# Kernel optimization log

Measured on AMD Instinct MI355X. Metric: run time of the kernel, lower is better.

The kernel has to match this reference:

```python
import jax, jax.numpy as jnp
import numpy as np

M = 2048      # tokens (batch*seq)
K = 4096      # infeatures
N = 4096      # outfeatures
G = 128       # quantization groupsize


def setup_inputs() -> dict:
    key = jax.random.key(0)
    k1, k2, k3 = jax.random.split(key, 3)
    x = jax.random.normal(k1, (M, K), dtype=jnp.float32)
    # Packed int4 weights: 8 nibbles per int32. Row block i holds output
    # features 8*i..8*i+7 for every input feature (tile=1 layout).
    B = jax.random.randint(k2, (N // 8, K), 0, 2**31 - 1, dtype=jnp.int32)
    # Per-group symmetric scales, shape (K//G, N); small positive values.
    s = jax.random.uniform(k3, (K // G, N), dtype=jnp.float32, minval=0.005, maxval=0.02)
    return {"x": x, "B": B, "s": s}


def reference(x, B, s):
    # Unpack 8 4-bit values per int32: nibble r of B[i, j] is weight
    # for output feature 8*i + r, input feature j.
    shifts = (jnp.arange(8, dtype=jnp.int32) * 4)
    nib = (B[:, None, :] >> shifts[None, :, None]) & 0xF        # (N//8, 8, K)
    w = nib.reshape(N, K).astype(jnp.float32) - 8.0              # symmetric: q - (maxq+1)/2
    # Scale for weight (n_idx, k_idx) is s[k_idx // G, n_idx].
    scale = jnp.repeat(s, G, axis=0).T                           # (N, K)
    w_dq = w * scale                                             # dequantized weight
    return x @ w_dq.T                                            # (M, N)
```

## Files before the change

kernel.cpp:

```cpp
#include <hip/hip_runtime.h>
#include <stdint.h>
#include <stddef.h>

#define MDIM 2048
#define KDIM 4096
#define NDIM 4096
#define NTILE 32

using i32x4  = __attribute__((ext_vector_type(4))) int;
using i32x16 = __attribute__((ext_vector_type(16))) int;
using c16    = __attribute__((ext_vector_type(16))) char;

#define QA 31.75f
#define QW 793.75f
#define OUT_SCALE 3.9680203e-5f

__device__ __forceinline__ int q8(float v) {
    float r = rintf(v);
    r = fmaxf(-127.f, fminf(127.f, r));
    return (int)r;
}

__global__ __launch_bounds__(256) void prep(const float* __restrict__ x,
                                            const int* __restrict__ Bq,
                                            const float* __restrict__ s,
                                            char* __restrict__ a8,
                                            char* __restrict__ w8) {
    const int b = blockIdx.x, tid = threadIdx.x;
    if (b < 2048) {
        size_t t = (size_t)b * 256 + tid;
        const float* p = x + t * 16;
        float4 v0 = *(const float4*)(p);
        float4 v1 = *(const float4*)(p + 4);
        float4 v2 = *(const float4*)(p + 8);
        float4 v3 = *(const float4*)(p + 12);
        c16 o;
        o[0]  = (char)q8(v0.x * QA); o[1]  = (char)q8(v0.y * QA);
        o[2]  = (char)q8(v0.z * QA); o[3]  = (char)q8(v0.w * QA);
        o[4]  = (char)q8(v1.x * QA); o[5]  = (char)q8(v1.y * QA);
        o[6]  = (char)q8(v1.z * QA); o[7]  = (char)q8(v1.w * QA);
        o[8]  = (char)q8(v2.x * QA); o[9]  = (char)q8(v2.y * QA);
        o[10] = (char)q8(v2.z * QA); o[11] = (char)q8(v2.w * QA);
        o[12] = (char)q8(v3.x * QA); o[13] = (char)q8(v3.y * QA);
        o[14] = (char)q8(v3.z * QA); o[15] = (char)q8(v3.w * QA);
        *(c16*)(a8 + t * 16) = o;
    } else {
        const int n8 = b - 2048;
        const int kc = tid;
        const int* p = Bq + (size_t)n8 * KDIM + kc * 16;
        int v[16];
        {
            int4 b0 = *(const int4*)(p);
            int4 b1 = *(const int4*)(p + 4);
            int4 b2 = *(const int4*)(p + 8);
            int4 b3 = *(const int4*)(p + 12);
            v[0]=b0.x; v[1]=b0.y; v[2]=b0.z; v[3]=b0.w;
            v[4]=b1.x; v[5]=b1.y; v[6]=b1.z; v[7]=b1.w;
            v[8]=b2.x; v[9]=b2.y; v[10]=b2.z; v[11]=b2.w;
            v[12]=b3.x; v[13]=b3.y; v[14]=b3.z; v[15]=b3.w;
        }
        const float* sp = s + (size_t)(kc >> 3) * NDIM + n8 * 8;
        float4 s0 = *(const float4*)(sp);
        float4 s1 = *(const float4*)(sp + 4);
        float scv[8] = { s0.x * QW, s0.y * QW, s0.z * QW, s0.w * QW,
                         s1.x * QW, s1.y * QW, s1.z * QW, s1.w * QW };
#pragma unroll
        for (int r = 0; r < 8; ++r) {
            const int sh = r * 4;
            const float sc = scv[r];
            c16 o;
#pragma unroll
            for (int e = 0; e < 16; ++e)
                o[e] = (char)q8((float)(((v[e] >> sh) & 0xF) - 8) * sc);
            *(c16*)(w8 + (size_t)(n8 * 8 + r) * KDIM + kc * 16) = o;
        }
    }
}

__device__ __forceinline__ void gload16(const char* g, char* l) {
    __builtin_amdgcn_global_load_lds(
        (const __attribute__((address_space(1))) uint32_t*)g,
        (__attribute__((address_space(3))) uint32_t*)l, 16, 0, 0);
}

__global__ __launch_bounds__(256, 2) void gemm_i8(const char* __restrict__ A,
                                                  const char* __restrict__ W,
                                                  float* __restrict__ C) {
    __shared__ __align__(16) char L[2][2][2][8192];

    const int tid  = threadIdx.x;
    const int lane = tid & 63;
    const int wave = tid >> 6;

    const int wg    = blockIdx.y * gridDim.x + blockIdx.x;
    const int xcd   = wg & 7;
    const int local = wg >> 3;
    const int bx    = xcd * 4 + (local & 3);
    const int by    = local >> 2;
    const int bm = by * 128;
    const int bn = bx * 128;

    const int wm = (wave >> 1) * 64;
    const int wn = (wave & 1) * 64;
    const int r32 = lane & 31;
    const int hi  = lane >> 5;

    const int sr0 = tid & 127,  sq0 = tid >> 7;
    const int sr1 = sr0,        sq1 = sq0 + 2;
    const size_t a0 = (size_t)(bm + sr0) * KDIM + sq0 * 16;
    const size_t a1 = (size_t)(bm + sr1) * KDIM + sq1 * 16;
    const size_t w0 = (size_t)(bn + sr0) * KDIM + sq0 * 16;
    const size_t w1 = (size_t)(bn + sr1) * KDIM + sq1 * 16;
    const int d0 = tid * 16, d1 = d0 + 4096;

    int asl[2][2], bsl[2][2];
#pragma unroll
    for (int i = 0; i < 2; i++)
#pragma unroll
        for (int kk = 0; kk < 2; kk++) {
            asl[i][kk] = (kk * 2 + hi) * 2048 + (wm + i * 32 + r32) * 16;
            bsl[i][kk] = (kk * 2 + hi) * 2048 + (wn + i * 32 + r32) * 16;
        }

    i32x16 acc[2][2] = {};

#define STAGE(SB, SK, KT) do {                                               \
        const size_t kb_ = (size_t)(KT) * 128 + (SK) * 64;                   \
        gload16(A + a0 + kb_, &L[SB][SK][0][d0]);                            \
        gload16(A + a1 + kb_, &L[SB][SK][0][d1]);                            \
        gload16(W + w0 + kb_, &L[SB][SK][1][d0]);                            \
        gload16(W + w1 + kb_, &L[SB][SK][1][d1]);                            \
    } while (0)

    STAGE(0, 0, 0);
    STAGE(0, 1, 0);
    asm volatile("s_waitcnt vmcnt(0)" ::: "memory");
    __builtin_amdgcn_s_barrier();

    for (int t = 0; t < NTILE; ++t) {
        const int buf = t & 1;
        const int nt  = (t + 1 < NTILE) ? t + 1 : NTILE - 1;
        const int nb  = (t + 1) & 1;
        STAGE(nb, 0, nt);
        STAGE(nb, 1, nt);

        i32x4 af[2][2][2], bf[2][2][2];
#pragma unroll
        for (int s = 0; s < 2; ++s) {
#pragma unroll
            for (int i = 0; i < 2; i++)
#pragma unroll
                for (int kk = 0; kk < 2; kk++) {
                    af[s][i][kk] = *(const i32x4*)&L[buf][s][0][asl[i][kk]];
                    bf[s][i][kk] = *(const i32x4*)&L[buf][s][1][bsl[i][kk]];
                }
        }

        __builtin_amdgcn_s_setprio(1);
#pragma unroll
        for (int s = 0; s < 2; ++s)
#pragma unroll
            for (int kk = 0; kk < 2; kk++)
#pragma unroll
                for (int i = 0; i < 2; i++)
#pragma unroll
                    for (int j = 0; j < 2; j++)
                        acc[i][j] = __builtin_amdgcn_mfma_i32_32x32x32_i8(
                            af[s][i][kk], bf[s][j][kk], acc[i][j], 0, 0, 0);
        __builtin_amdgcn_s_setprio(0);

        asm volatile("s_waitcnt vmcnt(0)" ::: "memory");
        __builtin_amdgcn_s_barrier();
    }
#undef STAGE

    const int colb = bn + wn + r32;
#pragma unroll
    for (int i = 0; i < 2; i++)
#pragma unroll
        for (int j = 0; j < 2; j++)
#pragma unroll
            for (int g = 0; g < 16; ++g) {
                const int row = bm + wm + i * 32 + (g & 3) + 8 * (g >> 2) + 4 * hi;
                C[(size_t)row * NDIM + (colb + j * 32)]
                    = (float)acc[i][j][g] * OUT_SCALE;
            }
}

extern "C" void kernel_launch(void* const* d_in, const int* in_sizes, int n_in,
                              void* d_out, int out_size, void* d_ws, size_t ws_size,
                              hipStream_t stream) {
    const float* x  = (const float*)d_in[0];
    const int*   Bq = (const int*)d_in[1];
    const float* s  = (const float*)d_in[2];
    float* out = (float*)d_out;

    char* a8 = (char*)d_ws;
    char* w8 = a8 + (size_t)MDIM * KDIM;

    hipLaunchKernelGGL(prep, dim3(2560), dim3(256), 0, stream,
                       x, Bq, s, a8, w8);
    hipLaunchKernelGGL(gemm_i8, dim3(NDIM / 128, MDIM / 128), dim3(256),
                       0, stream, a8, w8, out);
}
```

Baseline: 167.6 us.

## Pre-tile int8 operands into LDS-ready panel layout for contiguous GEMM loads

The prep kernel now writes quantized activations and weights in a tiled panel layout: 128-row panels split into 64-wide K slices, each an 8 KB block already laid out exactly as the GEMM's LDS staging expects. The GEMM then loads each slice with fully contiguous 16-byte global_load_lds accesses instead of strided row reads across a 4 KB row pitch. The aim is better DRAM/L2 access efficiency in the GEMM. In exchange, prep's activation stores and read pattern change, with fewer, heavier blocks, and its weight stores are scattered at 16-byte granularity.

```diff
diff --git a/kernel.cpp b/kernel.cpp
--- a/kernel.cpp
+++ b/kernel.cpp
@@ -27,25 +27,34 @@
                                             char* __restrict__ a8,
                                             char* __restrict__ w8) {
     const int b = blockIdx.x, tid = threadIdx.x;
-    if (b < 2048) {
-        size_t t = (size_t)b * 256 + tid;
-        const float* p = x + t * 16;
-        float4 v0 = *(const float4*)(p);
-        float4 v1 = *(const float4*)(p + 4);
-        float4 v2 = *(const float4*)(p + 8);
-        float4 v3 = *(const float4*)(p + 12);
-        c16 o;
-        o[0]  = (char)q8(v0.x * QA); o[1]  = (char)q8(v0.y * QA);
-        o[2]  = (char)q8(v0.z * QA); o[3]  = (char)q8(v0.w * QA);
-        o[4]  = (char)q8(v1.x * QA); o[5]  = (char)q8(v1.y * QA);
-        o[6]  = (char)q8(v1.z * QA); o[7]  = (char)q8(v1.w * QA);
-        o[8]  = (char)q8(v2.x * QA); o[9]  = (char)q8(v2.y * QA);
-        o[10] = (char)q8(v2.z * QA); o[11] = (char)q8(v2.w * QA);
-        o[12] = (char)q8(v3.x * QA); o[13] = (char)q8(v3.y * QA);
-        o[14] = (char)q8(v3.z * QA); o[15] = (char)q8(v3.w * QA);
-        *(c16*)(a8 + t * 16) = o;
+    if (b < 1024) {
+        const int p  = b >> 6;
+        const int sl = b & 63;
+        const int row = tid & 127;
+        const int q0  = tid >> 7;
+        const float* prow = x + (size_t)(p * 128 + row) * KDIM + sl * 64;
+        char* dst = a8 + (size_t)b * 8192;
+#pragma unroll
+        for (int h = 0; h < 2; ++h) {
+            const int q = q0 + h * 2;
+            const float* pp = prow + q * 16;
+            float4 v0 = *(const float4*)(pp);
+            float4 v1 = *(const float4*)(pp + 4);
+            float4 v2 = *(const float4*)(pp + 8);
+            float4 v3 = *(const float4*)(pp + 12);
+            c16 o;
+            o[0]  = (char)q8(v0.x * QA); o[1]  = (char)q8(v0.y * QA);
+            o[2]  = (char)q8(v0.z * QA); o[3]  = (char)q8(v0.w * QA);
+            o[4]  = (char)q8(v1.x * QA); o[5]  = (char)q8(v1.y * QA);
+            o[6]  = (char)q8(v1.z * QA); o[7]  = (char)q8(v1.w * QA);
+            o[8]  = (char)q8(v2.x * QA); o[9]  = (char)q8(v2.y * QA);
+            o[10] = (char)q8(v2.z * QA); o[11] = (char)q8(v2.w * QA);
+            o[12] = (char)q8(v3.x * QA); o[13] = (char)q8(v3.y * QA);
+            o[14] = (char)q8(v3.z * QA); o[15] = (char)q8(v3.w * QA);
+            *(c16*)(dst + (size_t)(q * 128 + row) * 16) = o;
+        }
     } else {
-        const int n8 = b - 2048;
+        const int n8 = b - 1024;
         const int kc = tid;
         const int* p = Bq + (size_t)n8 * KDIM + kc * 16;
         int v[16];
@@ -64,6 +73,10 @@
         float4 s1 = *(const float4*)(sp + 4);
         float scv[8] = { s0.x * QW, s0.y * QW, s0.z * QW, s0.w * QW,
                          s1.x * QW, s1.y * QW, s1.z * QW, s1.w * QW };
+        const int sl = kc >> 2, q = kc & 3;
+        char* dst = w8 + (size_t)(n8 >> 4) * 524288
+                       + (size_t)sl * 8192 + q * 2048
+                       + (size_t)((n8 & 15) * 8) * 16;
 #pragma unroll
         for (int r = 0; r < 8; ++r) {
             const int sh = r * 4;
@@ -72,7 +85,7 @@
 #pragma unroll
             for (int e = 0; e < 16; ++e)
                 o[e] = (char)q8((float)(((v[e] >> sh) & 0xF) - 8) * sc);
-            *(c16*)(w8 + (size_t)(n8 * 8 + r) * KDIM + kc * 16) = o;
+            *(c16*)(dst + r * 16) = o;
         }
     }
 }
@@ -105,12 +118,8 @@
     const int r32 = lane & 31;
     const int hi  = lane >> 5;
 
-    const int sr0 = tid & 127,  sq0 = tid >> 7;
-    const int sr1 = sr0,        sq1 = sq0 + 2;
-    const size_t a0 = (size_t)(bm + sr0) * KDIM + sq0 * 16;
-    const size_t a1 = (size_t)(bm + sr1) * KDIM + sq1 * 16;
-    const size_t w0 = (size_t)(bn + sr0) * KDIM + sq0 * 16;
-    const size_t w1 = (size_t)(bn + sr1) * KDIM + sq1 * 16;
+    const char* Apan = A + (size_t)by * 524288;
+    const char* Wpan = W + (size_t)bx * 524288;
     const int d0 = tid * 16, d1 = d0 + 4096;
 
     int asl[2][2], bsl[2][2];
@@ -124,16 +133,16 @@
 
     i32x16 acc[2][2] = {};
 
-#define STAGE(SB, SK, KT) do {                                               \
-        const size_t kb_ = (size_t)(KT) * 128 + (SK) * 64;                   \
-        gload16(A + a0 + kb_, &L[SB][SK][0][d0]);                            \
-        gload16(A + a1 + kb_, &L[SB][SK][0][d1]);                            \
-        gload16(W + w0 + kb_, &L[SB][SK][1][d0]);                            \
-        gload16(W + w1 + kb_, &L[SB][SK][1][d1]);                            \
+#define STAGE(SB, SK, SL) do {                                               \
+        const size_t so_ = (size_t)(SL) * 8192;                              \
+        gload16(Apan + so_ + d0, &L[SB][SK][0][d0]);                         \
+        gload16(Apan + so_ + d1, &L[SB][SK][0][d1]);                         \
+        gload16(Wpan + so_ + d0, &L[SB][SK][1][d0]);                         \
+        gload16(Wpan + so_ + d1, &L[SB][SK][1][d1]);                         \
     } while (0)
 
     STAGE(0, 0, 0);
-    STAGE(0, 1, 0);
+    STAGE(0, 1, 1);
     asm volatile("s_waitcnt vmcnt(0)" ::: "memory");
     __builtin_amdgcn_s_barrier();
 
@@ -141,8 +150,8 @@
         const int buf = t & 1;
         const int nt  = (t + 1 < NTILE) ? t + 1 : NTILE - 1;
         const int nb  = (t + 1) & 1;
-        STAGE(nb, 0, nt);
-        STAGE(nb, 1, nt);
+        STAGE(nb, 0, nt * 2);
+        STAGE(nb, 1, nt * 2 + 1);
 
         i32x4 af[2][2][2], bf[2][2][2];
 #pragma unroll
@@ -198,7 +207,7 @@
     char* a8 = (char*)d_ws;
     char* w8 = a8 + (size_t)MDIM * KDIM;
 
-    hipLaunchKernelGGL(prep, dim3(2560), dim3(256), 0, stream,
+    hipLaunchKernelGGL(prep, dim3(1536), dim3(256), 0, stream,
                        x, Bq, s, a8, w8);
     hipLaunchKernelGGL(gemm_i8, dim3(NDIM / 128, MDIM / 128), dim3(256),
                        0, stream, a8, w8, out);
```

New measurement: 135.9 us (median of 2 runs). 1.23x faster.
